# Kernel tuning notes

Measured on AMD Instinct MI355X. Metric: run time of the kernel, lower is better.

## Reference

```python
import math
import jax, jax.numpy as jnp
import numpy as np

EPS = 1e-6
N_HEAD = 12


def _rmsnorm(x, g):
    # x * rsqrt(mean(x^2, -1) + eps) * g  (computed in fp32 like the original)
    return x * jax.lax.rsqrt(jnp.mean(x * x, axis=-1, keepdims=True) + EPS) * g


def setup_inputs() -> dict:
    key = jax.random.key(0)
    B, T, C = 4, 1536, 768
    ks = jax.random.split(key, 12)
    s = 0.02

    def w(k, shape):
        return (jax.random.normal(k, shape) * s).astype(jnp.float32)

    return {
        "x": jax.random.normal(ks[0], (B, T, C), dtype=jnp.float32),
        "g1": jnp.ones((C,), jnp.float32),
        "g2": jnp.ones((C,), jnp.float32),
        "W_in": w(ks[1], (C, C)), "b_in": jnp.zeros((C,), jnp.float32),
        "W_act": w(ks[2], (C, C)), "b_act": jnp.zeros((C,), jnp.float32),
        "W_out": w(ks[3], (C, C)), "b_out": jnp.zeros((C,), jnp.float32),
        "Wq": w(ks[4], (C, C)), "bq": jnp.zeros((C,), jnp.float32),
        "Wk": w(ks[5], (C, C)), "bk": jnp.zeros((C,), jnp.float32),
        "Wv": w(ks[6], (C, C)), "bv": jnp.zeros((C,), jnp.float32),
        "Wp": w(ks[7], (C, C)), "bp": jnp.zeros((C,), jnp.float32),
        "W1": w(ks[8], (C, 4 * C)), "b1": jnp.zeros((4 * C,), jnp.float32),
        "W2": w(ks[9], (4 * C, C)), "b2": jnp.zeros((C,), jnp.float32),
    }


def reference(x, g1, g2, W_in, b_in, W_act, b_act, W_out, b_out,
              Wq, bq, Wk, bk, Wv, bv, Wp, bp, W1, b1, W2, b2):
    B, T, C = x.shape
    H = N_HEAD
    D = C // H
    t = T // 3

    shortcut = x
    h = _rmsnorm(x, g1)

    # gated dual projection
    act_res = jax.nn.silu(h @ W_act + b_act)          # [B,T,C]
    u = jax.nn.silu(h @ W_in + b_in)                  # [B,T,C]

    # block-causal self-attention on u
    q = (u @ Wq + bq).reshape(B, T, H, D).transpose(0, 2, 1, 3)  # [B,H,T,D]
    k = (u @ Wk + bk).reshape(B, T, H, D).transpose(0, 2, 1, 3)
    v = (u @ Wv + bv).reshape(B, T, H, D).transpose(0, 2, 1, 3)

    scale = 1.0 / math.sqrt(D)
    att = jnp.einsum('bhqd,bhkd->bhqk', q, k) * scale            # [B,H,T,T]
    # tril(t,t) tiled 3x3: position i attends j iff (j mod t) <= (i mod t)
    mask = jnp.tile(jnp.tril(jnp.ones((t, t), dtype=bool)), (3, 3))  # [T,T]
    att = jnp.where(mask, att, -jnp.inf)
    att = jax.nn.softmax(att, axis=-1)
    y = jnp.einsum('bhqk,bhkd->bhqd', att, v)                    # [B,H,T,D]
    y = y.transpose(0, 2, 1, 3).reshape(B, T, C)
    y = y @ Wp + bp                                              # attn out proj

    # gate + out projection + residual
    x = shortcut + (y * act_res) @ W_out + b_out

    # MLP (exact GELU, matching torch nn.GELU default)
    m = _rmsnorm(x, g2)
    x = x + jax.nn.gelu(m @ W1 + b1, approximate=False) @ W2 + b2
    return x
```

## Files before the change

### kernel.cpp

```cpp
#include <hip/hip_runtime.h>
#include <math.h>

#define B_SZ   4
#define T_SEQ  1536
#define C_DIM  768
#define QKVC   (3 * C_DIM)
#define NH     12
#define HD     64
#define TBLK   512
#define M_ROWS (B_SZ * T_SEQ)
#define NQT    12
#define NFLAT  (B_SZ * NH * NQT)

#define ACT_NONE 0
#define ACT_SILU 1
#define ACT_GELU 2
#define OUT_BF16 8
#define OUT_DUAL 16

typedef __attribute__((ext_vector_type(8))) short bf16x8;
typedef __attribute__((ext_vector_type(4))) float f32x4;

#define WAITCNT_VM(n) asm volatile("s_waitcnt vmcnt(" #n ")" ::: "memory")
#define WAITCNT_LGKM0 asm volatile("s_waitcnt lgkmcnt(0)" ::: "memory")

static __device__ __forceinline__ void gload_lds16(const void* g, void* l) {
    __builtin_amdgcn_global_load_lds(
        (const __attribute__((address_space(1))) void*)g,
        (__attribute__((address_space(3))) void*)l, 16, 0, 0);
}

static __device__ __forceinline__ unsigned short f2bf(float f) {
    unsigned int u = __float_as_uint(f);
    u += 0x7fffu + ((u >> 16) & 1u);
    return (unsigned short)(u >> 16);
}

struct WPtrs { const float* p[7]; };

__global__ __launch_bounds__(256) void wtrans7_kernel(WPtrs w, unsigned short* out) {
    __shared__ float t[32][33];
    const int tx = threadIdx.x, ty = threadIdx.y;
    const int n0 = blockIdx.x * 32, k0 = blockIdx.y * 32;
    const float* in = w.p[blockIdx.z];
    unsigned short* o = out + (size_t)blockIdx.z * C_DIM * C_DIM;
    #pragma unroll
    for (int j = 0; j < 4; ++j)
        t[ty + 8 * j][tx] = in[(size_t)(k0 + ty + 8 * j) * C_DIM + n0 + tx];
    __syncthreads();
    #pragma unroll
    for (int j = 0; j < 4; ++j)
        o[(size_t)(n0 + ty + 8 * j) * C_DIM + k0 + tx] = f2bf(t[tx][ty + 8 * j]);
}

__global__ __launch_bounds__(256) void wtrans_kernel(const float* in, unsigned short* out, int K, int N) {
    __shared__ float t[32][33];
    const int tx = threadIdx.x, ty = threadIdx.y;
    const int n0 = blockIdx.x * 32, k0 = blockIdx.y * 32;
    #pragma unroll
    for (int j = 0; j < 4; ++j)
        t[ty + 8 * j][tx] = in[(size_t)(k0 + ty + 8 * j) * N + n0 + tx];
    __syncthreads();
    #pragma unroll
    for (int j = 0; j < 4; ++j)
        out[(size_t)(n0 + ty + 8 * j) * K + k0 + tx] = f2bf(t[tx][ty + 8 * j]);
}

__global__ __launch_bounds__(256) void biascat_kernel(const float* bq, const float* bk, const float* bv,
                                                      const float* ba, const float* bi,
                                                      float* qkvb, float* actb) {
    const int i = blockIdx.x * 256 + threadIdx.x;
    if (i < 2304) qkvb[i] = (i < 768) ? bq[i] : ((i < 1536) ? bk[i - 768] : bv[i - 1536]);
    if (i < 1536) actb[i] = (i < 768) ? ba[i] : bi[i - 768];
}

__global__ __launch_bounds__(256) void vtrans_kernel(const unsigned short* in, unsigned short* out) {
    __shared__ unsigned short t[32][33];
    const int tx = threadIdx.x, ty = threadIdx.y;
    const int t0 = blockIdx.x * 32;
    const int d0 = blockIdx.y * 32;
    const int z  = blockIdx.z;
    const int b  = z / NH, h = z % NH;
    #pragma unroll
    for (int j = 0; j < 4; ++j)
        t[ty + 8 * j][tx] = in[((size_t)b * T_SEQ + t0 + ty + 8 * j) * QKVC + 2 * C_DIM + h * HD + d0 + tx];
    __syncthreads();
    #pragma unroll
    for (int j = 0; j < 4; ++j)
        out[((size_t)z * HD + d0 + ty + 8 * j) * T_SEQ + t0 + tx] = t[tx][ty + 8 * j];
}

__global__ __launch_bounds__(256) void rmsnorm_kernel(const float* x, const float* g, unsigned short* out) {
    const int row = blockIdx.x;
    const int tid = threadIdx.x;
    const float* xr = x + (size_t)row * C_DIM;

    const float v0 = xr[tid];
    const float v1 = xr[tid + 256];
    const float v2 = xr[tid + 512];
    float ss = v0 * v0 + v1 * v1 + v2 * v2;

    #pragma unroll
    for (int off = 32; off > 0; off >>= 1) ss += __shfl_xor(ss, off, 64);
    __shared__ float s_red[4];
    if ((tid & 63) == 0) s_red[tid >> 6] = ss;
    __syncthreads();
    ss = s_red[0] + s_red[1] + s_red[2] + s_red[3];

    const float r = rsqrtf(ss * (1.0f / C_DIM) + 1e-6f);
    unsigned short* orow = out + (size_t)row * C_DIM;
    orow[tid]       = f2bf(v0 * r * g[tid]);
    orow[tid + 256] = f2bf(v1 * r * g[tid + 256]);
    orow[tid + 512] = f2bf(v2 * r * g[tid + 512]);
}

template<int TBM, int TBN>
__global__ __launch_bounds__(256) void gemm_t(const unsigned short* A, const unsigned short* Bt,
                                              const float* bias, const float* gmul, const float* resid,
                                              void* outp, int M, int N, int K, int mode) {
    constexpr int WN  = (TBM == 128) ? 2 : 4;
    constexpr int WNC = TBN / WN;
    constexpr int FM  = 4;
    constexpr int FN  = WNC / 16;
    constexpr int NA  = TBM / 8;
    constexpr int NB  = TBN / 8;
    constexpr int LA  = NA / 4, LB = NB / 4;
    constexpr int LPT = LA + LB;

    __shared__ unsigned short As[2][TBM * 64];
    __shared__ unsigned short Bs[2][TBN * 64];

    const int tid  = threadIdx.x;
    const int lane = tid & 63;
    const int wid  = tid >> 6;
    const int wr   = wid / WN;
    const int wc   = wid % WN;
    const int m0   = blockIdx.x * TBM;
    const int n0   = blockIdx.y * TBN;

    const int l15 = lane & 15;
    const int l4  = lane >> 4;

    const int lrow = lane >> 3;
    const int csw  = (((lane & 7) ^ lrow) << 4);

    f32x4 acc[FM][FN] = {};

    const char* Ab = (const char*)A;
    const char* Bb = (const char*)Bt;

    auto stage = [&](int buf, int k0) {
        char* Ad = (char*)&As[buf][0];
        char* Bd = (char*)&Bs[buf][0];
        #pragma unroll
        for (int j = 0; j < LA; ++j) {
            const int chunk = wid * LA + j;
            const int row   = chunk * 8 + lrow;
            gload_lds16(Ab + ((size_t)(m0 + row) * K + k0) * 2 + csw, Ad + chunk * 1024);
        }
        #pragma unroll
        for (int j = 0; j < LB; ++j) {
            const int chunk = wid * LB + j;
            const int row   = chunk * 8 + lrow;
            gload_lds16(Bb + ((size_t)(n0 + row) * K + k0) * 2 + csw, Bd + chunk * 1024);
        }
    };

    stage(0, 0);
    int cur = 0;
    for (int k0 = 0; k0 < K; k0 += 64) {
        if (k0 + 64 < K) {
            stage(cur ^ 1, k0 + 64);
            if constexpr (LPT == 8) { WAITCNT_VM(8); } else { WAITCNT_VM(6); }
        } else {
            WAITCNT_VM(0);
        }
        __builtin_amdgcn_s_barrier();
        __builtin_amdgcn_sched_barrier(0);

        const unsigned short* Ac = &As[cur][0];
        const unsigned short* Bc = &Bs[cur][0];
        #pragma unroll
        for (int kk = 0; kk < 2; ++kk) {
            bf16x8 af[FM], bfr[FN];
            const int g = l4 + 4 * kk;
            #pragma unroll
            for (int fm = 0; fm < FM; ++fm)
                af[fm] = *(const bf16x8*)&Ac[(wr * 64 + fm * 16 + l15) * 64 + ((g ^ (l15 & 7)) * 8)];
            #pragma unroll
            for (int fn = 0; fn < FN; ++fn)
                bfr[fn] = *(const bf16x8*)&Bc[(wc * WNC + fn * 16 + l15) * 64 + ((g ^ (l15 & 7)) * 8)];
            #pragma unroll
            for (int fm = 0; fm < FM; ++fm)
                #pragma unroll
                for (int fn = 0; fn < FN; ++fn)
                    acc[fm][fn] = __builtin_amdgcn_mfma_f32_16x16x32_bf16(
                        af[fm], bfr[fn], acc[fm][fn], 0, 0, 0);
        }

        WAITCNT_LGKM0;
        __builtin_amdgcn_s_barrier();
        cur ^= 1;
    }

    const int act = mode & 7;
    #pragma unroll
    for (int fm = 0; fm < FM; ++fm) {
        #pragma unroll
        for (int r = 0; r < 4; ++r) {
            const int m = m0 + wr * 64 + fm * 16 + l4 * 4 + r;
            #pragma unroll
            for (int fn = 0; fn < FN; ++fn) {
                const int n = n0 + wc * WNC + fn * 16 + l15;
                float v = acc[fm][fn][r];
                if (bias) v += bias[n];
                if (act == ACT_SILU) {
                    v = v / (1.0f + expf(-v));
                } else if (act == ACT_GELU) {
                    v = 0.5f * v * (1.0f + erff(v * 0.70710678118654752f));
                }
                if (mode & OUT_DUAL) {
                    if (n < 768) ((float*)gmul)[(size_t)m * 768 + n] = v;
                    else ((unsigned short*)outp)[(size_t)m * 768 + (n - 768)] = f2bf(v);
                } else {
                    if (gmul)  v *= gmul[(size_t)m * N + n];
                    if (resid) v += resid[(size_t)m * N + n];
                    if (mode & OUT_BF16) ((unsigned short*)outp)[(size_t)m * N + n] = f2bf(v);
                    else                 ((float*)outp)[(size_t)m * N + n] = v;
                }
            }
        }
    }
}

#define PPITCH 72

__global__ __launch_bounds__(256) void attn_mfma(const unsigned short* qkv, const unsigned short* vt,
                                                 float* Opart, float* mpart, float* lpart) {
    __shared__ unsigned short Qs[128 * 64];
    __shared__ unsigned short Ks[2][64 * 64];
    __shared__ unsigned short Vs[2][64 * 64];
    __shared__ unsigned short Pl[128 * PPITCH];

    const int tid  = threadIdx.x;
    const int lane = tid & 63;
    const int w    = tid >> 6;
    const int l15  = lane & 15;
    const int l4   = lane >> 4;
    const int qt   = blockIdx.x;
    const int h    = blockIdx.y;
    const int b    = blockIdx.z / 3;
    const int kb   = blockIdx.z % 3;
    const int i0   = qt * 128;
    const int qb   = qt & 3;

    const size_t bT = (size_t)b * T_SEQ;
    const unsigned short* qp = qkv + bT * QKVC + h * HD;
    const unsigned short* kp = qkv + bT * QKVC + C_DIM + h * HD;
    const size_t vtb = (size_t)(b * NH + h) * HD * T_SEQ;
    const int flat = (b * NH + h) * NQT + qt;

    const int lr   = lane >> 3;
    const int csrc = ((lane & 7) ^ lr) * 8;

    #pragma unroll
    for (int i = 0; i < 4; ++i) {
        const int row = w * 32 + i * 8 + lr;
        gload_lds16(qp + (size_t)(i0 + row) * QKVC + csrc,
                    (char*)Qs + (w * 32 + i * 8) * 128);
    }

    auto stage_kv = [&](int buf, int jt) {
        const int j0 = kb * TBLK + jt * 64;
        #pragma unroll
        for (int i = 0; i < 2; ++i) {
            const int row = w * 8 + i * 32 + lr;
            gload_lds16(kp + (size_t)(j0 + row) * QKVC + csrc,
                        (char*)&Ks[buf][0] + (w * 8 + i * 32) * 128);
            gload_lds16(vt + vtb + (size_t)row * T_SEQ + j0 + csrc,
                        (char*)&Vs[buf][0] + (w * 8 + i * 32) * 128);
        }
    };

    f32x4 o[2][4] = {};
    float m_run[2][4], l_run[2][4];
    #pragma unroll
    for (int a = 0; a < 2; ++a)
        #pragma unroll
        for (int r = 0; r < 4; ++r) { m_run[a][r] = -INFINITY; l_run[a][r] = 0.f; }

    const int jt_max = 2 * qb + 1;
    stage_kv(0, 0);
    int cur = 0;
    for (int jt = 0; jt <= jt_max; ++jt) {
        const bool diag = (jt >= 2 * qb);

        if (jt < jt_max) {
            stage_kv(cur ^ 1, jt + 1);
            WAITCNT_VM(4);
        } else {
            WAITCNT_VM(0);
        }
        __builtin_amdgcn_s_barrier();
        __builtin_amdgcn_sched_barrier(0);

        f32x4 s[2][4] = {};
        #pragma unroll
        for (int kk = 0; kk < 2; ++kk) {
            bf16x8 af[2], bfr[4];
            #pragma unroll
            for (int a = 0; a < 2; ++a)
                af[a] = *(const bf16x8*)&Qs[(w * 32 + a * 16 + l15) * 64 + (((l4 + 4 * kk) ^ (l15 & 7)) * 8)];
            #pragma unroll
            for (int n = 0; n < 4; ++n)
                bfr[n] = *(const bf16x8*)&Ks[cur][(n * 16 + l15) * 64 + (((l4 + 4 * kk) ^ (l15 & 7)) * 8)];
            #pragma unroll
            for (int a = 0; a < 2; ++a)
                #pragma unroll
                for (int n = 0; n < 4; ++n)
                    s[a][n] = __builtin_amdgcn_mfma_f32_16x16x32_bf16(af[a], bfr[n], s[a][n], 0, 0, 0);
        }

        #pragma unroll
        for (int a = 0; a < 2; ++a) {
            #pragma unroll
            for (int r = 0; r < 4; ++r) {
                const int imod = qb * 128 + w * 32 + a * 16 + l4 * 4 + r;
                float pv[4];
                float rowm = -INFINITY;
                #pragma unroll
                for (int n = 0; n < 4; ++n) {
                    float sv = s[a][n][r] * 0.125f;
                    if (diag) {
                        const int jmod = jt * 64 + n * 16 + l15;
                        if (jmod > imod) sv = -INFINITY;
                    }
                    pv[n] = sv;
                    rowm = fmaxf(rowm, sv);
                }
                #pragma unroll
                for (int off = 1; off < 16; off <<= 1) rowm = fmaxf(rowm, __shfl_xor(rowm, off, 64));
                const float mn = fmaxf(m_run[a][r], rowm);
                const float sc = __expf(m_run[a][r] - mn);
                float rs = 0.f;
                #pragma unroll
                for (int n = 0; n < 4; ++n) {
                    const float e = __expf(pv[n] - mn);
                    pv[n] = e;
                    rs += e;
                }
                #pragma unroll
                for (int off = 1; off < 16; off <<= 1) rs += __shfl_xor(rs, off, 64);
                l_run[a][r] = l_run[a][r] * sc + rs;
                m_run[a][r] = mn;
                const int qrow = w * 32 + a * 16 + l4 * 4 + r;
                #pragma unroll
                for (int n = 0; n < 4; ++n) {
                    o[a][n][r] *= sc;
                    Pl[qrow * PPITCH + n * 16 + l15] = f2bf(pv[n]);
                }
            }
        }
        WAITCNT_LGKM0;
        __builtin_amdgcn_s_barrier();
        __builtin_amdgcn_sched_barrier(0);

        #pragma unroll
        for (int kk = 0; kk < 2; ++kk) {
            bf16x8 af[2], bfr[4];
            #pragma unroll
            for (int a = 0; a < 2; ++a)
                af[a] = *(const bf16x8*)&Pl[(w * 32 + a * 16 + l15) * PPITCH + l4 * 8 + kk * 32];
            #pragma unroll
            for (int n = 0; n < 4; ++n)
                bfr[n] = *(const bf16x8*)&Vs[cur][(n * 16 + l15) * 64 + (((l4 + 4 * kk) ^ (l15 & 7)) * 8)];
            #pragma unroll
            for (int a = 0; a < 2; ++a)
                #pragma unroll
                for (int n = 0; n < 4; ++n)
                    o[a][n] = __builtin_amdgcn_mfma_f32_16x16x32_bf16(af[a], bfr[n], o[a][n], 0, 0, 0);
        }

        WAITCNT_LGKM0;
        __builtin_amdgcn_s_barrier();
        __builtin_amdgcn_sched_barrier(0);
        cur ^= 1;
    }

    float* Ob = Opart + ((size_t)kb * NFLAT + flat) * (128 * 64);
    #pragma unroll
    for (int a = 0; a < 2; ++a) {
        #pragma unroll
        for (int r = 0; r < 4; ++r) {
            const int qq = w * 32 + a * 16 + l4 * 4 + r;
            #pragma unroll
            for (int n = 0; n < 4; ++n)
                Ob[(size_t)qq * 64 + n * 16 + l15] = o[a][n][r];
            if (l15 == 0) {
                mpart[((size_t)kb * NFLAT + flat) * 128 + qq] = m_run[a][r];
                lpart[((size_t)kb * NFLAT + flat) * 128 + qq] = l_run[a][r];
            }
        }
    }
}

__global__ __launch_bounds__(256) void attn_merge(const float* Opart, const float* mpart, const float* lpart,
                                                  unsigned short* y) {
    const int flat = blockIdx.x;
    const int qt = flat % NQT;
    const int h  = (flat / NQT) % NH;
    const int b  = flat / (NQT * NH);
    const int t  = threadIdx.x;
    const int r  = t >> 1;
    const int c0 = (t & 1) * 32;

    const size_t rowoff = (size_t)flat * 128 + r;
    float m0 = mpart[0 * (size_t)NFLAT * 128 + rowoff];
    float m1 = mpart[1 * (size_t)NFLAT * 128 + rowoff];
    float m2 = mpart[2 * (size_t)NFLAT * 128 + rowoff];
    const float ms = fmaxf(fmaxf(m0, m1), m2);
    const float w0 = __expf(m0 - ms), w1 = __expf(m1 - ms), w2 = __expf(m2 - ms);
    const float ls = lpart[0 * (size_t)NFLAT * 128 + rowoff] * w0 +
                     lpart[1 * (size_t)NFLAT * 128 + rowoff] * w1 +
                     lpart[2 * (size_t)NFLAT * 128 + rowoff] * w2;
    const float inv = 1.0f / ls;

    const size_t obase = ((size_t)flat * 128 + r) * 64 + c0;
    const float* O0 = Opart + 0 * (size_t)NFLAT * 128 * 64 + obase;
    const float* O1 = Opart + 1 * (size_t)NFLAT * 128 * 64 + obase;
    const float* O2 = Opart + 2 * (size_t)NFLAT * 128 * 64 + obase;

    unsigned short* yp = y + ((size_t)b * T_SEQ + qt * 128 + r) * C_DIM + h * HD + c0;
    #pragma unroll
    for (int j = 0; j < 8; ++j) {
        const float4 a = *reinterpret_cast<const float4*>(O0 + j * 4);
        const float4 bq = *reinterpret_cast<const float4*>(O1 + j * 4);
        const float4 cq = *reinterpret_cast<const float4*>(O2 + j * 4);
        ushort4 ov;
        ov.x = f2bf((a.x * w0 + bq.x * w1 + cq.x * w2) * inv);
        ov.y = f2bf((a.y * w0 + bq.y * w1 + cq.y * w2) * inv);
        ov.z = f2bf((a.z * w0 + bq.z * w1 + cq.z * w2) * inv);
        ov.w = f2bf((a.w * w0 + bq.w * w1 + cq.w * w2) * inv);
        *reinterpret_cast<ushort4*>(yp + j * 4) = ov;
    }
}

extern "C" void kernel_launch(void* const* d_in, const int* in_sizes, int n_in,
                              void* d_out, int out_size, void* d_ws, size_t ws_size,
                              hipStream_t stream) {
    const float* x     = (const float*)d_in[0];
    const float* g1    = (const float*)d_in[1];
    const float* g2    = (const float*)d_in[2];
    const float* W_in  = (const float*)d_in[3];
    const float* b_in  = (const float*)d_in[4];
    const float* W_act = (const float*)d_in[5];
    const float* b_act = (const float*)d_in[6];
    const float* W_out = (const float*)d_in[7];
    const float* b_out = (const float*)d_in[8];
    const float* Wq    = (const float*)d_in[9];
    const float* bq    = (const float*)d_in[10];
    const float* Wk    = (const float*)d_in[11];
    const float* bk    = (const float*)d_in[12];
    const float* Wv    = (const float*)d_in[13];
    const float* bv    = (const float*)d_in[14];
    const float* Wp    = (const float*)d_in[15];
    const float* bp    = (const float*)d_in[16];
    const float* W1    = (const float*)d_in[17];
    const float* b1    = (const float*)d_in[18];
    const float* W2    = (const float*)d_in[19];
    const float* b2    = (const float*)d_in[20];
    float* out = (float*)d_out;

    const float* FNULL = 0;

    float* ws = (float*)d_ws;
    unsigned short* wsb = (unsigned short*)d_ws;
    const size_t U = (size_t)M_ROWS * C_DIM;

    unsigned short* wt = wsb;
    float* qkvb    = ws + 4500000;
    float* actb    = ws + 4505000;
    float* act_res = ws + 1 * U;
    unsigned short* h_bf   = wsb + 4 * U;
    unsigned short* u_bf   = wsb + 5 * U;
    unsigned short* qkv_bf = wsb + 6 * U;
    unsigned short* vt_bf  = wsb + 9 * U;
    unsigned short* y_bf   = wsb + 4 * U;
    unsigned short* g_bf   = wsb + 5 * U;
    float*          x1     = ws  + 3 * U;
    unsigned short* m_bf   = wsb + 8 * U;
    unsigned short* a1_bf  = wsb + 9 * U;
    float* Opart = ws + 5 * U;
    float* mpart = ws + 8 * U;
    float* lpart = ws + 8 * U + (size_t)3 * NFLAT * 128;

    const size_t WCC = (size_t)C_DIM * C_DIM;
    unsigned short* Wt_actin = wt;
    unsigned short* Wt_qkv   = wt + 2 * WCC;
    unsigned short* Wtp      = wt + 5 * WCC;
    unsigned short* Wt_out   = wt + 6 * WCC;
    unsigned short* Wt1      = wt + 7 * WCC;
    unsigned short* Wt2      = Wt1 + (size_t)C_DIM * 4 * C_DIM;

    const dim3 tb(32, 8);
    WPtrs wp;
    wp.p[0] = W_act; wp.p[1] = W_in; wp.p[2] = Wq; wp.p[3] = Wk;
    wp.p[4] = Wv;    wp.p[5] = Wp;   wp.p[6] = W_out;
    wtrans7_kernel<<<dim3(24, 24, 7), tb, 0, stream>>>(wp, wt);
    wtrans_kernel<<<dim3(4 * C_DIM / 32, C_DIM / 32), tb, 0, stream>>>(W1, Wt1, C_DIM, 4 * C_DIM);
    wtrans_kernel<<<dim3(C_DIM / 32, 4 * C_DIM / 32), tb, 0, stream>>>(W2, Wt2, 4 * C_DIM, C_DIM);
    biascat_kernel<<<9, 256, 0, stream>>>(bq, bk, bv, b_act, b_in, qkvb, actb);

    const dim3 blk(256);
    const dim3 g_actin(M_ROWS / 128, 1536 / 128);
    const dim3 g_qkv(M_ROWS / 128, QKVC / 128);
    const dim3 g_cc64(M_ROWS / 64, C_DIM / 128);
    const dim3 g_c4(M_ROWS / 128, 4 * C_DIM / 128);
    const dim3 g_vt(T_SEQ / 32, HD / 32, B_SZ * NH);
    const dim3 g_attn(NQT, NH, B_SZ * 3);

    rmsnorm_kernel<<<M_ROWS, blk, 0, stream>>>(x, g1, h_bf);
    gemm_t<128,128><<<g_actin, blk, 0, stream>>>(h_bf, Wt_actin, actb, act_res, FNULL,
                                                 (void*)u_bf, M_ROWS, 1536, C_DIM,
                                                 ACT_SILU | OUT_BF16 | OUT_DUAL);
    gemm_t<128,128><<<g_qkv, blk, 0, stream>>>(u_bf, Wt_qkv, qkvb, FNULL, FNULL,
                                               (void*)qkv_bf, M_ROWS, QKVC, C_DIM, ACT_NONE | OUT_BF16);
    vtrans_kernel<<<g_vt, tb, 0, stream>>>(qkv_bf, vt_bf);
    attn_mfma<<<g_attn, blk, 0, stream>>>(qkv_bf, vt_bf, Opart, mpart, lpart);
    attn_merge<<<NFLAT, blk, 0, stream>>>(Opart, mpart, lpart, y_bf);
    gemm_t<64,128><<<g_cc64, blk, 0, stream>>>(y_bf, Wtp, bp, act_res, FNULL,
                                               (void*)g_bf, M_ROWS, C_DIM, C_DIM, ACT_NONE | OUT_BF16);
    gemm_t<64,128><<<g_cc64, blk, 0, stream>>>(g_bf, Wt_out, b_out, FNULL, x,
                                               (void*)x1, M_ROWS, C_DIM, C_DIM, ACT_NONE);
    rmsnorm_kernel<<<M_ROWS, blk, 0, stream>>>(x1, g2, m_bf);
    gemm_t<128,128><<<g_c4, blk, 0, stream>>>(m_bf, Wt1, b1, FNULL, FNULL,
                                              (void*)a1_bf, M_ROWS, 4 * C_DIM, C_DIM, ACT_GELU | OUT_BF16);
    gemm_t<64,128><<<g_cc64, blk, 0, stream>>>(a1_bf, Wt2, b2, FNULL, x1,
                                               (void*)out, M_ROWS, C_DIM, 4 * C_DIM, ACT_NONE);
}
```

Before: 699.9 us.

## Single-buffer GEMM LDS with launch bounds 4 and fast SiLU/GELU epilogues

Drops the double-buffered LDS prefetch pipeline in the GEMM in favor of a single buffer with plain syncthreads around each K-step. This halves shared memory, and together with __launch_bounds__(256,4) is meant to raise occupancy so that other waves hide load latency. It also swaps expf/erff in the epilogue for hardware rcp/exp and an Abramowitz-Stegun erf polynomial, which cuts epilogue cost at a small accuracy cost. Losing the explicit overlap of global loads with MFMA work may stall each block.

Result: faster. 601.9 us (-14.0%).

```diff
diff --git a/kernel.cpp b/kernel.cpp
--- a/kernel.cpp
+++ b/kernel.cpp
@@ -36,6 +36,21 @@
     return (unsigned short)(u >> 16);
 }
 
+static __device__ __forceinline__ float silu_f(float x) {
+    return x * __builtin_amdgcn_rcpf(1.0f + __expf(-x));
+}
+
+static __device__ __forceinline__ float gelu_f(float x) {
+    const float ax = fabsf(x) * 0.70710678118654752f;
+    const float t  = __builtin_amdgcn_rcpf(1.0f + 0.3275911f * ax);
+    const float e  = __expf(-ax * ax);
+    float p = ((((1.061405429f * t - 1.453152027f) * t) + 1.421413741f) * t
+               - 0.284496736f) * t + 0.254829592f;
+    float erfv = 1.0f - p * t * e;
+    erfv = (x < 0.f) ? -erfv : erfv;
+    return 0.5f * x * (1.0f + erfv);
+}
+
 struct WPtrs { const float* p[7]; };
 
 __global__ __launch_bounds__(256) void wtrans7_kernel(WPtrs w, unsigned short* out) {
@@ -114,21 +129,20 @@
     orow[tid + 512] = f2bf(v2 * r * g[tid + 512]);
 }
 
-template<int TBM, int TBN>
-__global__ __launch_bounds__(256) void gemm_t(const unsigned short* A, const unsigned short* Bt,
-                                              const float* bias, const float* gmul, const float* resid,
-                                              void* outp, int M, int N, int K, int mode) {
+template<int TBM>
+__global__ __launch_bounds__(256, 4) void gemm_t(const unsigned short* A, const unsigned short* Bt,
+                                                 const float* bias, const float* gmul, const float* resid,
+                                                 void* outp, int M, int N, int K, int mode) {
+    constexpr int TBN = 128;
     constexpr int WN  = (TBM == 128) ? 2 : 4;
     constexpr int WNC = TBN / WN;
     constexpr int FM  = 4;
     constexpr int FN  = WNC / 16;
-    constexpr int NA  = TBM / 8;
-    constexpr int NB  = TBN / 8;
-    constexpr int LA  = NA / 4, LB = NB / 4;
-    constexpr int LPT = LA + LB;
-
-    __shared__ unsigned short As[2][TBM * 64];
-    __shared__ unsigned short Bs[2][TBN * 64];
+    constexpr int LA  = TBM / 32;
+    constexpr int LB  = 4;
+
+    __shared__ unsigned short As[TBM * 64];
+    __shared__ unsigned short Bs[TBN * 64];
 
     const int tid  = threadIdx.x;
     const int lane = tid & 63;
@@ -149,47 +163,32 @@
     const char* Ab = (const char*)A;
     const char* Bb = (const char*)Bt;
 
-    auto stage = [&](int buf, int k0) {
-        char* Ad = (char*)&As[buf][0];
-        char* Bd = (char*)&Bs[buf][0];
+    for (int k0 = 0; k0 < K; k0 += 64) {
+        __syncthreads();
         #pragma unroll
         for (int j = 0; j < LA; ++j) {
             const int chunk = wid * LA + j;
             const int row   = chunk * 8 + lrow;
-            gload_lds16(Ab + ((size_t)(m0 + row) * K + k0) * 2 + csw, Ad + chunk * 1024);
+            gload_lds16(Ab + ((size_t)(m0 + row) * K + k0) * 2 + csw, (char*)As + chunk * 1024);
         }
         #pragma unroll
         for (int j = 0; j < LB; ++j) {
             const int chunk = wid * LB + j;
             const int row   = chunk * 8 + lrow;
-            gload_lds16(Bb + ((size_t)(n0 + row) * K + k0) * 2 + csw, Bd + chunk * 1024);
-        }
-    };
-
-    stage(0, 0);
-    int cur = 0;
-    for (int k0 = 0; k0 < K; k0 += 64) {
-        if (k0 + 64 < K) {
-            stage(cur ^ 1, k0 + 64);
-            if constexpr (LPT == 8) { WAITCNT_VM(8); } else { WAITCNT_VM(6); }
-        } else {
-            WAITCNT_VM(0);
-        }
-        __builtin_amdgcn_s_barrier();
-        __builtin_amdgcn_sched_barrier(0);
-
-        const unsigned short* Ac = &As[cur][0];
-        const unsigned short* Bc = &Bs[cur][0];
+            gload_lds16(Bb + ((size_t)(n0 + row) * K + k0) * 2 + csw, (char*)Bs + chunk * 1024);
+        }
+        __syncthreads();
+
         #pragma unroll
         for (int kk = 0; kk < 2; ++kk) {
             bf16x8 af[FM], bfr[FN];
             const int g = l4 + 4 * kk;
             #pragma unroll
             for (int fm = 0; fm < FM; ++fm)
-                af[fm] = *(const bf16x8*)&Ac[(wr * 64 + fm * 16 + l15) * 64 + ((g ^ (l15 & 7)) * 8)];
+                af[fm] = *(const bf16x8*)&As[(wr * 64 + fm * 16 + l15) * 64 + ((g ^ (l15 & 7)) * 8)];
             #pragma unroll
             for (int fn = 0; fn < FN; ++fn)
-                bfr[fn] = *(const bf16x8*)&Bc[(wc * WNC + fn * 16 + l15) * 64 + ((g ^ (l15 & 7)) * 8)];
+                bfr[fn] = *(const bf16x8*)&Bs[(wc * WNC + fn * 16 + l15) * 64 + ((g ^ (l15 & 7)) * 8)];
             #pragma unroll
             for (int fm = 0; fm < FM; ++fm)
                 #pragma unroll
@@ -197,10 +196,6 @@
                     acc[fm][fn] = __builtin_amdgcn_mfma_f32_16x16x32_bf16(
                         af[fm], bfr[fn], acc[fm][fn], 0, 0, 0);
         }
-
-        WAITCNT_LGKM0;
-        __builtin_amdgcn_s_barrier();
-        cur ^= 1;
     }
 
     const int act = mode & 7;
@@ -214,11 +209,8 @@
                 const int n = n0 + wc * WNC + fn * 16 + l15;
                 float v = acc[fm][fn][r];
                 if (bias) v += bias[n];
-                if (act == ACT_SILU) {
-                    v = v / (1.0f + expf(-v));
-                } else if (act == ACT_GELU) {
-                    v = 0.5f * v * (1.0f + erff(v * 0.70710678118654752f));
-                }
+                if (act == ACT_SILU)      v = silu_f(v);
+                else if (act == ACT_GELU) v = gelu_f(v);
                 if (mode & OUT_DUAL) {
                     if (n < 768) ((float*)gmul)[(size_t)m * 768 + n] = v;
                     else ((unsigned short*)outp)[(size_t)m * 768 + (n - 768)] = f2bf(v);
@@ -520,21 +512,21 @@
     const dim3 g_attn(NQT, NH, B_SZ * 3);
 
     rmsnorm_kernel<<<M_ROWS, blk, 0, stream>>>(x, g1, h_bf);
-    gemm_t<128,128><<<g_actin, blk, 0, stream>>>(h_bf, Wt_actin, actb, act_res, FNULL,
-                                                 (void*)u_bf, M_ROWS, 1536, C_DIM,
-                                                 ACT_SILU | OUT_BF16 | OUT_DUAL);
-    gemm_t<128,128><<<g_qkv, blk, 0, stream>>>(u_bf, Wt_qkv, qkvb, FNULL, FNULL,
-                                               (void*)qkv_bf, M_ROWS, QKVC, C_DIM, ACT_NONE | OUT_BF16);
+    gemm_t<128><<<g_actin, blk, 0, stream>>>(h_bf, Wt_actin, actb, act_res, FNULL,
+                                             (void*)u_bf, M_ROWS, 1536, C_DIM,
+                                             ACT_SILU | OUT_BF16 | OUT_DUAL);
+    gemm_t<128><<<g_qkv, blk, 0, stream>>>(u_bf, Wt_qkv, qkvb, FNULL, FNULL,
+                                           (void*)qkv_bf, M_ROWS, QKVC, C_DIM, ACT_NONE | OUT_BF16);
     vtrans_kernel<<<g_vt, tb, 0, stream>>>(qkv_bf, vt_bf);
     attn_mfma<<<g_attn, blk, 0, stream>>>(qkv_bf, vt_bf, Opart, mpart, lpart);
     attn_merge<<<NFLAT, blk, 0, stream>>>(Opart, mpart, lpart, y_bf);
-    gemm_t<64,128><<<g_cc64, blk, 0, stream>>>(y_bf, Wtp, bp, act_res, FNULL,
-                                               (void*)g_bf, M_ROWS, C_DIM, C_DIM, ACT_NONE | OUT_BF16);
-    gemm_t<64,128><<<g_cc64, blk, 0, stream>>>(g_bf, Wt_out, b_out, FNULL, x,
-                                               (void*)x1, M_ROWS, C_DIM, C_DIM, ACT_NONE);
+    gemm_t<64><<<g_cc64, blk, 0, stream>>>(y_bf, Wtp, bp, act_res, FNULL,
+                                           (void*)g_bf, M_ROWS, C_DIM, C_DIM, ACT_NONE | OUT_BF16);
+    gemm_t<64><<<g_cc64, blk, 0, stream>>>(g_bf, Wt_out, b_out, FNULL, x,
+                                           (void*)x1, M_ROWS, C_DIM, C_DIM, ACT_NONE);
     rmsnorm_kernel<<<M_ROWS, blk, 0, stream>>>(x1, g2, m_bf);
-    gemm_t<128,128><<<g_c4, blk, 0, stream>>>(m_bf, Wt1, b1, FNULL, FNULL,
-                                              (void*)a1_bf, M_ROWS, 4 * C_DIM, C_DIM, ACT_GELU | OUT_BF16);
-    gemm_t<64,128><<<g_cc64, blk, 0, stream>>>(a1_bf, Wt2, b2, FNULL, x1,
-                                               (void*)out, M_ROWS, C_DIM, 4 * C_DIM, ACT_NONE);
-}
+    gemm_t<128><<<g_c4, blk, 0, stream>>>(m_bf, Wt1, b1, FNULL, FNULL,
+                                          (void*)a1_bf, M_ROWS, 4 * C_DIM, C_DIM, ACT_GELU | OUT_BF16);
+    gemm_t<64><<<g_cc64, blk, 0, stream>>>(a1_bf, Wt2, b2, FNULL, x1,
+                                           (void*)out, M_ROWS, C_DIM, 4 * C_DIM, ACT_NONE);
+}
```
